# Kernel tuning notes

Hardware: AMD Instinct MI355X
Metric: run time of the kernel (lower is better)

Reference implementation:

```python
import jax, jax.numpy as jnp
import numpy as np

MSA_DIM = 256
N_HEADS = 8
HEAD_DIM = MSA_DIM // N_HEADS
PAIR_DIM = 128
SCALE = 1.0 / float(np.sqrt(HEAD_DIM))


def setup_inputs() -> dict:
    key = jax.random.key(0)
    ks = jax.random.split(key, 7)
    B, S, L = 1, 128, 384
    return {
        "msa": jax.random.normal(ks[0], (B, S, L, MSA_DIM), dtype=jnp.float32),
        "pair": jax.random.normal(ks[1], (B, L, L, PAIR_DIM), dtype=jnp.float32),
        "Wq": jax.random.normal(ks[2], (MSA_DIM, MSA_DIM), dtype=jnp.float32) * 0.02,
        "Wk": jax.random.normal(ks[3], (MSA_DIM, MSA_DIM), dtype=jnp.float32) * 0.02,
        "Wv": jax.random.normal(ks[4], (MSA_DIM, MSA_DIM), dtype=jnp.float32) * 0.02,
        "Wo": jax.random.normal(ks[5], (MSA_DIM, MSA_DIM), dtype=jnp.float32) * 0.02,
        "Wpb": jax.random.normal(ks[6], (N_HEADS, PAIR_DIM), dtype=jnp.float32) * 0.02,
    }


def reference(msa, pair, Wq, Wk, Wv, Wo, Wpb):
    B, S, L, D = msa.shape
    H, hd = N_HEADS, HEAD_DIM
    # projections (nn.Linear: y = x @ W.T), split heads -> (B,S,H,L,hd)
    q = (msa @ Wq.T).reshape(B, S, L, H, hd)
    k = (msa @ Wk.T).reshape(B, S, L, H, hd)
    v = (msa @ Wv.T).reshape(B, S, L, H, hd)
    # NOTE: faithful to the original forward — pair_bias is computed but the
    # Triton kernel performs plain flash attention, so the bias is NOT added.
    _pair_bias = jnp.einsum('bijp,hp->bhij', pair, Wpb)  # dead code, as in source
    # attention logits per MSA row: (B,S,H,L,L)
    scores = jnp.einsum('bslhd,bsmhd->bshlm', q, k) * SCALE
    attn = jax.nn.softmax(scores, axis=-1)
    out = jnp.einsum('bshlm,bsmhd->bslhd', attn, v).reshape(B, S, L, D)
    return out @ Wo.T
```

## Files before the change

### kernel.cpp

```cpp
#include <hip/hip_runtime.h>
#include <stdint.h>

typedef unsigned short u16;
typedef __bf16 bf16x8 __attribute__((ext_vector_type(8)));
typedef short s16x4 __attribute__((ext_vector_type(4)));
typedef float f32x4 __attribute__((ext_vector_type(4)));

#define QKV_STRIDE 12288

__device__ __forceinline__ u16 f2bf(float x) {
    unsigned int u = __float_as_uint(x);
    u += 0x7fffu + ((u >> 16) & 1u);
    return (u16)(u >> 16);
}
__device__ __forceinline__ float bf2f(u16 h) {
    return __uint_as_float(((unsigned int)h) << 16);
}

__device__ __forceinline__ void async_copy16(const u16* g, u16* l) {
    __builtin_amdgcn_global_load_lds(
        (const __attribute__((address_space(1))) unsigned int*)g,
        (__attribute__((address_space(3))) unsigned int*)l, 16, 0, 0);
}

static __device__ __forceinline__ f32x4 pv_mfma(s16x4 a, s16x4 b, f32x4 c) {
#if __has_builtin(__builtin_amdgcn_mfma_f32_16x16x16bf16_1k)
    return __builtin_amdgcn_mfma_f32_16x16x16bf16_1k(a, b, c, 0, 0, 0);
#else
    union { s16x4 h[2]; bf16x8 v; } ua, ub;
    s16x4 zz = {0, 0, 0, 0};
    ua.h[0] = a; ua.h[1] = zz;
    ub.h[0] = b; ub.h[1] = zz;
    return __builtin_amdgcn_mfma_f32_16x16x32_bf16(ua.v, ub.v, c, 0, 0, 0);
#endif
}

__global__ void prep(const float* __restrict__ msa,
                     const float* __restrict__ Wq, const float* __restrict__ Wk,
                     const float* __restrict__ Wv, const float* __restrict__ Wo,
                     u16* __restrict__ msa_bf, u16* __restrict__ Wqkv,
                     u16* __restrict__ Woh, u16* __restrict__ Wol) {
    int b = blockIdx.x;
    if (b < 12288) {
        int i = b * 256 + threadIdx.x;
        float4 v = ((const float4*)msa)[i];
        ushort4 o;
        o.x = f2bf(v.x); o.y = f2bf(v.y); o.z = f2bf(v.z); o.w = f2bf(v.w);
        ((ushort4*)msa_bf)[i] = o;
    } else {
        int i = (b - 12288) * 256 + threadIdx.x;
        Wqkv[i]          = f2bf(Wq[i]);
        Wqkv[65536 + i]  = f2bf(Wk[i]);
        Wqkv[131072 + i] = f2bf(Wv[i]);
        float w = Wo[i];
        u16 hi = f2bf(w);
        Woh[i] = hi;
        Wol[i] = f2bf(w - bf2f(hi));
    }
}

__launch_bounds__(256, 2)
__global__ void qkv_gemm(const u16* __restrict__ A, const u16* __restrict__ W,
                         u16* __restrict__ Qb, u16* __restrict__ Kb, u16* __restrict__ VTb) {
    __shared__ __align__(16) u16 As[128 * 32];
    __shared__ __align__(16) u16 Bs[128 * 32];
    const int tid = threadIdx.x;
    const int tm = blockIdx.x % 384, tn = blockIdx.x / 384;
    const bool trans = (tn < 4);
    const int lane = tid & 63, wave = tid >> 6;
    const int lm = lane & 15, lq = lane >> 4;
    const int wm = (wave >> 1) * 64, wn = (wave & 1) * 64;
    const float CEXPF = 0.17677669529663687f * 1.4426950408889634f;
    f32x4 acc[4][4] = {};

    const int srow = wave * 16 + (lane >> 2);
    const int scol = (lane & 3) * 8;
    u16* ldsA0 = &As[wave * 512 + lane * 8];
    u16* ldsA1 = &As[2048 + wave * 512 + lane * 8];
    u16* ldsB0 = &Bs[wave * 512 + lane * 8];
    u16* ldsB1 = &Bs[2048 + wave * 512 + lane * 8];
    const u16* gA0 = &A[(tm * 128 + srow) * 256 + scol];
    const u16* gA1 = &A[(tm * 128 + 64 + srow) * 256 + scol];
    const u16* gB0 = &W[(tn * 128 + srow) * 256 + scol];
    const u16* gB1 = &W[(tn * 128 + 64 + srow) * 256 + scol];

    for (int k0 = 0; k0 < 256; k0 += 32) {
        async_copy16(gA0 + k0, ldsA0);
        async_copy16(gA1 + k0, ldsA1);
        async_copy16(gB0 + k0, ldsB0);
        async_copy16(gB1 + k0, ldsB1);
        __syncthreads();
        const u16* Xs = trans ? Bs : As;
        const u16* Ys = trans ? As : Bs;
        bf16x8 xf[4], yf[4];
        #pragma unroll
        for (int i = 0; i < 4; ++i)
            xf[i] = *(const bf16x8*)&Xs[(wm + i * 16 + lm) * 32 + lq * 8];
        #pragma unroll
        for (int j = 0; j < 4; ++j)
            yf[j] = *(const bf16x8*)&Ys[(wn + j * 16 + lm) * 32 + lq * 8];
        #pragma unroll
        for (int i = 0; i < 4; ++i)
            #pragma unroll
            for (int j = 0; j < 4; ++j)
                acc[i][j] = __builtin_amdgcn_mfma_f32_16x16x32_bf16(xf[i], yf[j], acc[i][j], 0, 0, 0);
        __syncthreads();
    }

    if (trans) {
        #pragma unroll
        for (int i = 0; i < 4; ++i) {
            int F0 = tn * 128 + wm + i * 16 + lq * 4;
            int which = F0 >> 8;
            int h = (F0 >> 5) & 7, d0 = F0 & 31;
            u16* dst = which ? Kb : Qb;
            float scale = which ? 1.0f : CEXPF;
            #pragma unroll
            for (int j = 0; j < 4; ++j) {
                int R = tm * 128 + wn + j * 16 + lm;
                int s = R / 384, l = R - s * 384;
                ushort4 o;
                o.x = f2bf(acc[i][j][0] * scale);
                o.y = f2bf(acc[i][j][1] * scale);
                o.z = f2bf(acc[i][j][2] * scale);
                o.w = f2bf(acc[i][j][3] * scale);
                *(ushort4*)&dst[((s * 8 + h) * 384 + l) * 32 + d0] = o;
            }
        }
    } else {
        #pragma unroll
        for (int j = 0; j < 4; ++j) {
            int F = tn * 128 + wn + j * 16 + lm;
            int h = (F >> 5) & 7, d = F & 31;
            #pragma unroll
            for (int i = 0; i < 4; ++i) {
                int R0 = tm * 128 + wm + i * 16 + lq * 4;
                int s = R0 / 384, l0 = R0 - s * 384;
                ushort4 o;
                o.x = f2bf(acc[i][j][0]);
                o.y = f2bf(acc[i][j][1]);
                o.z = f2bf(acc[i][j][2]);
                o.w = f2bf(acc[i][j][3]);
                *(ushort4*)&VTb[((s * 8 + h) * 32 + d) * 384 + l0] = o;
            }
        }
    }
}

__launch_bounds__(256, 6)
__global__ void msa_attention(const u16* __restrict__ Qb, const u16* __restrict__ Kb,
                              const u16* __restrict__ VTb,
                              u16* __restrict__ Ahi, u16* __restrict__ Alo) {
    __shared__ __align__(16) u16 Vt[32 * 392];
    const int tid = threadIdx.x;
    const int bid = blockIdx.x;
    const int sh = bid / 3, lpart = bid - sh * 3;
    const int s = sh >> 3, h = sh & 7;
    const u16* Qg = Qb + (size_t)sh * QKV_STRIDE;
    const u16* Kg = Kb + (size_t)sh * QKV_STRIDE;
    const u16* Vg = VTb + (size_t)sh * QKV_STRIDE;

    for (int i = tid; i < 1536; i += 256) {
        int d = i / 48, c = i - d * 48;
        *(uint4*)&Vt[d * 392 + c * 8] = *(const uint4*)&Vg[d * 384 + c * 8];
    }

    const int lane = tid & 63, wave = tid >> 6;
    const int lm = lane & 15, lq = lane >> 4;

    bf16x8 aq[2];
    #pragma unroll
    for (int it = 0; it < 2; ++it) {
        int l = lpart * 128 + (wave * 2 + it) * 16 + lm;
        aq[it] = *(const bf16x8*)&Qg[l * 32 + lq * 8];
    }
    __syncthreads();

    f32x4 o[2][2] = {};
    f32x4 lacc[2] = {};
    const s16x4 ones = {(short)0x3F80, (short)0x3F80, (short)0x3F80, (short)0x3F80};

    for (int n0 = 0; n0 < 384; n0 += 32) {
        bf16x8 kf0 = *(const bf16x8*)&Kg[(n0 + lm) * 32 + lq * 8];
        bf16x8 kf1 = *(const bf16x8*)&Kg[(n0 + 16 + lm) * 32 + lq * 8];
        s16x4 vf00 = *(const s16x4*)&Vt[lm * 392 + n0 + lq * 4];
        s16x4 vf01 = *(const s16x4*)&Vt[lm * 392 + n0 + 16 + lq * 4];
        s16x4 vf10 = *(const s16x4*)&Vt[(16 + lm) * 392 + n0 + lq * 4];
        s16x4 vf11 = *(const s16x4*)&Vt[(16 + lm) * 392 + n0 + 16 + lq * 4];
        #pragma unroll
        for (int it = 0; it < 2; ++it) {
            f32x4 z = {0.f, 0.f, 0.f, 0.f};
            f32x4 s0 = __builtin_amdgcn_mfma_f32_16x16x32_bf16(kf0, aq[it], z, 0, 0, 0);
            f32x4 s1 = __builtin_amdgcn_mfma_f32_16x16x32_bf16(kf1, aq[it], z, 0, 0, 0);
            float p0[4], p1[4];
            #pragma unroll
            for (int r = 0; r < 4; ++r) {
                p0[r] = __builtin_amdgcn_exp2f(s0[r]);
                p1[r] = __builtin_amdgcn_exp2f(s1[r]);
            }
            union { s16x4 v; uint2 u; } pk0, pk1;
            pk0.u.x = __builtin_amdgcn_perm(__float_as_uint(p0[1]), __float_as_uint(p0[0]), 0x07060302u);
            pk0.u.y = __builtin_amdgcn_perm(__float_as_uint(p0[3]), __float_as_uint(p0[2]), 0x07060302u);
            pk1.u.x = __builtin_amdgcn_perm(__float_as_uint(p1[1]), __float_as_uint(p1[0]), 0x07060302u);
            pk1.u.y = __builtin_amdgcn_perm(__float_as_uint(p1[3]), __float_as_uint(p1[2]), 0x07060302u);
            o[it][0] = pv_mfma(vf00, pk0.v, o[it][0]);
            o[it][0] = pv_mfma(vf01, pk1.v, o[it][0]);
            o[it][1] = pv_mfma(vf10, pk0.v, o[it][1]);
            o[it][1] = pv_mfma(vf11, pk1.v, o[it][1]);
            lacc[it] = pv_mfma(ones, pk0.v, lacc[it]);
            lacc[it] = pv_mfma(ones, pk1.v, lacc[it]);
        }
    }

    #pragma unroll
    for (int it = 0; it < 2; ++it) {
        float inv = __builtin_amdgcn_rcpf(lacc[it][0]);
        int l = lpart * 128 + (wave * 2 + it) * 16 + lm;
        int base = (s * 384 + l) * 256 + h * 32 + lq * 4;
        #pragma unroll
        for (int dt = 0; dt < 2; ++dt) {
            ushort4 oh, ol;
            float x0 = o[it][dt][0] * inv, x1 = o[it][dt][1] * inv;
            float x2 = o[it][dt][2] * inv, x3 = o[it][dt][3] * inv;
            oh.x = f2bf(x0); ol.x = f2bf(x0 - bf2f(oh.x));
            oh.y = f2bf(x1); ol.y = f2bf(x1 - bf2f(oh.y));
            oh.z = f2bf(x2); ol.z = f2bf(x2 - bf2f(oh.z));
            oh.w = f2bf(x3); ol.w = f2bf(x3 - bf2f(oh.w));
            *(ushort4*)&Ahi[base + dt * 16] = oh;
            *(ushort4*)&Alo[base + dt * 16] = ol;
        }
    }
}

__launch_bounds__(256, 2)
__global__ void out_gemm(const u16* __restrict__ Ahi, const u16* __restrict__ Alo,
                         const u16* __restrict__ Woh, const u16* __restrict__ Wol,
                         float* __restrict__ out) {
    __shared__ __align__(16) u16 Ah[128 * 32], Al[128 * 32], Bh[128 * 32], Bl[128 * 32];
    const int tid = threadIdx.x;
    const int tm = blockIdx.x % 384, tn = blockIdx.x / 384;
    const int lane = tid & 63, wave = tid >> 6;
    const int lm = lane & 15, lq = lane >> 4;
    const int wm = (wave >> 1) * 64, wn = (wave & 1) * 64;
    f32x4 acc[4][4] = {};

    const int srow = wave * 16 + (lane >> 2);
    const int scol = (lane & 3) * 8;
    const int lo0 = wave * 512 + lane * 8, lo1 = 2048 + wave * 512 + lane * 8;
    const u16* gAh0 = &Ahi[(tm * 128 + srow) * 256 + scol];
    const u16* gAh1 = &Ahi[(tm * 128 + 64 + srow) * 256 + scol];
    const u16* gAl0 = &Alo[(tm * 128 + srow) * 256 + scol];
    const u16* gAl1 = &Alo[(tm * 128 + 64 + srow) * 256 + scol];
    const u16* gBh0 = &Woh[(tn * 128 + srow) * 256 + scol];
    const u16* gBh1 = &Woh[(tn * 128 + 64 + srow) * 256 + scol];
    const u16* gBl0 = &Wol[(tn * 128 + srow) * 256 + scol];
    const u16* gBl1 = &Wol[(tn * 128 + 64 + srow) * 256 + scol];

    for (int k0 = 0; k0 < 256; k0 += 32) {
        async_copy16(gAh0 + k0, &Ah[lo0]);
        async_copy16(gAh1 + k0, &Ah[lo1]);
        async_copy16(gAl0 + k0, &Al[lo0]);
        async_copy16(gAl1 + k0, &Al[lo1]);
        async_copy16(gBh0 + k0, &Bh[lo0]);
        async_copy16(gBh1 + k0, &Bh[lo1]);
        async_copy16(gBl0 + k0, &Bl[lo0]);
        async_copy16(gBl1 + k0, &Bl[lo1]);
        __syncthreads();
        bf16x8 whf[4], wlf[4], ahf[4], alf[4];
        #pragma unroll
        for (int i = 0; i < 4; ++i) {
            whf[i] = *(const bf16x8*)&Bh[(wm + i * 16 + lm) * 32 + lq * 8];
            wlf[i] = *(const bf16x8*)&Bl[(wm + i * 16 + lm) * 32 + lq * 8];
        }
        #pragma unroll
        for (int j = 0; j < 4; ++j) {
            ahf[j] = *(const bf16x8*)&Ah[(wn + j * 16 + lm) * 32 + lq * 8];
            alf[j] = *(const bf16x8*)&Al[(wn + j * 16 + lm) * 32 + lq * 8];
        }
        #pragma unroll
        for (int i = 0; i < 4; ++i)
            #pragma unroll
            for (int j = 0; j < 4; ++j) {
                acc[i][j] = __builtin_amdgcn_mfma_f32_16x16x32_bf16(whf[i], alf[j], acc[i][j], 0, 0, 0);
                acc[i][j] = __builtin_amdgcn_mfma_f32_16x16x32_bf16(wlf[i], ahf[j], acc[i][j], 0, 0, 0);
                acc[i][j] = __builtin_amdgcn_mfma_f32_16x16x32_bf16(whf[i], ahf[j], acc[i][j], 0, 0, 0);
            }
        __syncthreads();
    }
    #pragma unroll
    for (int i = 0; i < 4; ++i) {
        int F0 = tn * 128 + wm + i * 16 + lq * 4;
        #pragma unroll
        for (int j = 0; j < 4; ++j) {
            int R = tm * 128 + wn + j * 16 + lm;
            *(f32x4*)&out[R * 256 + F0] = acc[i][j];
        }
    }
}

extern "C" void kernel_launch(void* const* d_in, const int* in_sizes, int n_in,
                              void* d_out, int out_size, void* d_ws, size_t ws_size,
                              hipStream_t stream) {
    const float* msa = (const float*)d_in[0];
    const float* Wq = (const float*)d_in[2];
    const float* Wk = (const float*)d_in[3];
    const float* Wv = (const float*)d_in[4];
    const float* Wo = (const float*)d_in[5];
    char* ws = (char*)d_ws;
    u16* msa_bf = (u16*)(ws + 0);
    u16* Qb     = (u16*)(ws + 25165824);
    u16* Kb     = (u16*)(ws + 50331648);
    u16* VTb    = (u16*)(ws + 75497472);
    u16* Ahi    = (u16*)(ws + 100663296);
    u16* Alo    = (u16*)(ws + 125829120);
    u16* Wqkv   = (u16*)(ws + 150994944);
    u16* Woh    = (u16*)(ws + 151388160);
    u16* Wol    = (u16*)(ws + 151519232);
    float* out  = (float*)d_out;

    hipLaunchKernelGGL(prep, dim3(12544), dim3(256), 0, stream, msa, Wq, Wk, Wv, Wo,
                       msa_bf, Wqkv, Woh, Wol);
    hipLaunchKernelGGL(qkv_gemm, dim3(2304), dim3(256), 0, stream, msa_bf, Wqkv, Qb, Kb, VTb);
    hipLaunchKernelGGL(msa_attention, dim3(3072), dim3(256), 0, stream, Qb, Kb, VTb, Ahi, Alo);
    hipLaunchKernelGGL(out_gemm, dim3(768), dim3(256), 0, stream, Ahi, Alo, Woh, Wol, out);
}
```

Measured before the change: 264.8 us.

## Drop attention low-precision split, load weights directly to registers, swizzle LDS tiles

The attention output is now stored only as a single bf16 value, with no hi/lo split. This halves the attention write traffic and the out_gemm A-operand reads, and drops one MFMA per tile in out_gemm. Both GEMMs now stage only the activation tile in LDS, using a 64-wide K step and an XOR-swizzled layout to avoid bank conflicts. Weight fragments are loaded straight from global memory into registers. The attention kernel double-buffers the K and V fragments across the unrolled key loop and lowers its occupancy hint from 6 to 4. Accuracy drops slightly because the attention output residual is no longer kept.

```diff
diff --git a/kernel.cpp b/kernel.cpp
--- a/kernel.cpp
+++ b/kernel.cpp
@@ -62,48 +62,53 @@
 __launch_bounds__(256, 2)
 __global__ void qkv_gemm(const u16* __restrict__ A, const u16* __restrict__ W,
                          u16* __restrict__ Qb, u16* __restrict__ Kb, u16* __restrict__ VTb) {
-    __shared__ __align__(16) u16 As[128 * 32];
-    __shared__ __align__(16) u16 Bs[128 * 32];
+    __shared__ __align__(16) u16 As[128 * 64];
     const int tid = threadIdx.x;
     const int tm = blockIdx.x % 384, tn = blockIdx.x / 384;
     const bool trans = (tn < 4);
     const int lane = tid & 63, wave = tid >> 6;
     const int lm = lane & 15, lq = lane >> 4;
+    const int lm7 = lm & 7;
     const int wm = (wave >> 1) * 64, wn = (wave & 1) * 64;
     const float CEXPF = 0.17677669529663687f * 1.4426950408889634f;
     f32x4 acc[4][4] = {};
 
-    const int srow = wave * 16 + (lane >> 2);
-    const int scol = (lane & 3) * 8;
-    u16* ldsA0 = &As[wave * 512 + lane * 8];
-    u16* ldsA1 = &As[2048 + wave * 512 + lane * 8];
-    u16* ldsB0 = &Bs[wave * 512 + lane * 8];
-    u16* ldsB1 = &Bs[2048 + wave * 512 + lane * 8];
-    const u16* gA0 = &A[(tm * 128 + srow) * 256 + scol];
-    const u16* gA1 = &A[(tm * 128 + 64 + srow) * 256 + scol];
-    const u16* gB0 = &W[(tn * 128 + srow) * 256 + scol];
-    const u16* gB1 = &W[(tn * 128 + 64 + srow) * 256 + scol];
-
-    for (int k0 = 0; k0 < 256; k0 += 32) {
-        async_copy16(gA0 + k0, ldsA0);
-        async_copy16(gA1 + k0, ldsA1);
-        async_copy16(gB0 + k0, ldsB0);
-        async_copy16(gB1 + k0, ldsB1);
+    const int srow = wave * 8 + (lane >> 3);
+    const int schunk = (lane & 7) ^ (lane >> 3);
+    u16* ldsd[4]; const u16* gsrc[4];
+    #pragma unroll
+    for (int j = 0; j < 4; ++j) {
+        ldsd[j] = &As[j * 2048 + wave * 512 + lane * 8];
+        gsrc[j] = &A[(tm * 128 + j * 32 + srow) * 256 + schunk * 8];
+    }
+    const int rbm = trans ? wn : wm;
+    const int rbg = tn * 128 + (trans ? wm : wn);
+
+    for (int k0 = 0; k0 < 256; k0 += 64) {
+        #pragma unroll
+        for (int j = 0; j < 4; ++j) async_copy16(gsrc[j] + k0, ldsd[j]);
+        bf16x8 wf[4][2];
+        #pragma unroll
+        for (int x = 0; x < 4; ++x)
+            #pragma unroll
+            for (int kk = 0; kk < 2; ++kk)
+                wf[x][kk] = *(const bf16x8*)&W[(rbg + x * 16 + lm) * 256 + k0 + kk * 32 + lq * 8];
         __syncthreads();
-        const u16* Xs = trans ? Bs : As;
-        const u16* Ys = trans ? As : Bs;
-        bf16x8 xf[4], yf[4];
-        #pragma unroll
-        for (int i = 0; i < 4; ++i)
-            xf[i] = *(const bf16x8*)&Xs[(wm + i * 16 + lm) * 32 + lq * 8];
-        #pragma unroll
-        for (int j = 0; j < 4; ++j)
-            yf[j] = *(const bf16x8*)&Ys[(wn + j * 16 + lm) * 32 + lq * 8];
-        #pragma unroll
-        for (int i = 0; i < 4; ++i)
-            #pragma unroll
-            for (int j = 0; j < 4; ++j)
-                acc[i][j] = __builtin_amdgcn_mfma_f32_16x16x32_bf16(xf[i], yf[j], acc[i][j], 0, 0, 0);
+        bf16x8 mf[4][2];
+        #pragma unroll
+        for (int x = 0; x < 4; ++x)
+            #pragma unroll
+            for (int kk = 0; kk < 2; ++kk)
+                mf[x][kk] = *(const bf16x8*)&As[(rbm + x * 16 + lm) * 64 + ((kk * 4 + lq) ^ lm7) * 8];
+        #pragma unroll
+        for (int kk = 0; kk < 2; ++kk)
+            #pragma unroll
+            for (int i = 0; i < 4; ++i)
+                #pragma unroll
+                for (int j = 0; j < 4; ++j)
+                    acc[i][j] = __builtin_amdgcn_mfma_f32_16x16x32_bf16(
+                        trans ? wf[i][kk] : mf[i][kk],
+                        trans ? mf[j][kk] : wf[j][kk], acc[i][j], 0, 0, 0);
         __syncthreads();
     }
 
@@ -147,10 +152,9 @@
     }
 }
 
-__launch_bounds__(256, 6)
+__launch_bounds__(256, 4)
 __global__ void msa_attention(const u16* __restrict__ Qb, const u16* __restrict__ Kb,
-                              const u16* __restrict__ VTb,
-                              u16* __restrict__ Ahi, u16* __restrict__ Alo) {
+                              const u16* __restrict__ VTb, u16* __restrict__ Ahi) {
     __shared__ __align__(16) u16 Vt[32 * 392];
     const int tid = threadIdx.x;
     const int bid = blockIdx.x;
@@ -174,24 +178,38 @@
         int l = lpart * 128 + (wave * 2 + it) * 16 + lm;
         aq[it] = *(const bf16x8*)&Qg[l * 32 + lq * 8];
     }
+
+    bf16x8 kf0[2], kf1[2];
+    kf0[0] = *(const bf16x8*)&Kg[lm * 32 + lq * 8];
+    kf1[0] = *(const bf16x8*)&Kg[(16 + lm) * 32 + lq * 8];
     __syncthreads();
+    s16x4 vf[2][4];
+    vf[0][0] = *(const s16x4*)&Vt[lm * 392 + lq * 4];
+    vf[0][1] = *(const s16x4*)&Vt[lm * 392 + 16 + lq * 4];
+    vf[0][2] = *(const s16x4*)&Vt[(16 + lm) * 392 + lq * 4];
+    vf[0][3] = *(const s16x4*)&Vt[(16 + lm) * 392 + 16 + lq * 4];
 
     f32x4 o[2][2] = {};
     f32x4 lacc[2] = {};
     const s16x4 ones = {(short)0x3F80, (short)0x3F80, (short)0x3F80, (short)0x3F80};
 
-    for (int n0 = 0; n0 < 384; n0 += 32) {
-        bf16x8 kf0 = *(const bf16x8*)&Kg[(n0 + lm) * 32 + lq * 8];
-        bf16x8 kf1 = *(const bf16x8*)&Kg[(n0 + 16 + lm) * 32 + lq * 8];
-        s16x4 vf00 = *(const s16x4*)&Vt[lm * 392 + n0 + lq * 4];
-        s16x4 vf01 = *(const s16x4*)&Vt[lm * 392 + n0 + 16 + lq * 4];
-        s16x4 vf10 = *(const s16x4*)&Vt[(16 + lm) * 392 + n0 + lq * 4];
-        s16x4 vf11 = *(const s16x4*)&Vt[(16 + lm) * 392 + n0 + 16 + lq * 4];
+    #pragma unroll
+    for (int t = 0; t < 12; ++t) {
+        const int cur = t & 1, nxt = cur ^ 1;
+        if (t < 11) {
+            const int nn = (t + 1) * 32;
+            kf0[nxt] = *(const bf16x8*)&Kg[(nn + lm) * 32 + lq * 8];
+            kf1[nxt] = *(const bf16x8*)&Kg[(nn + 16 + lm) * 32 + lq * 8];
+            vf[nxt][0] = *(const s16x4*)&Vt[lm * 392 + nn + lq * 4];
+            vf[nxt][1] = *(const s16x4*)&Vt[lm * 392 + nn + 16 + lq * 4];
+            vf[nxt][2] = *(const s16x4*)&Vt[(16 + lm) * 392 + nn + lq * 4];
+            vf[nxt][3] = *(const s16x4*)&Vt[(16 + lm) * 392 + nn + 16 + lq * 4];
+        }
         #pragma unroll
         for (int it = 0; it < 2; ++it) {
             f32x4 z = {0.f, 0.f, 0.f, 0.f};
-            f32x4 s0 = __builtin_amdgcn_mfma_f32_16x16x32_bf16(kf0, aq[it], z, 0, 0, 0);
-            f32x4 s1 = __builtin_amdgcn_mfma_f32_16x16x32_bf16(kf1, aq[it], z, 0, 0, 0);
+            f32x4 s0 = __builtin_amdgcn_mfma_f32_16x16x32_bf16(kf0[cur], aq[it], z, 0, 0, 0);
+            f32x4 s1 = __builtin_amdgcn_mfma_f32_16x16x32_bf16(kf1[cur], aq[it], z, 0, 0, 0);
             float p0[4], p1[4];
             #pragma unroll
             for (int r = 0; r < 4; ++r) {
@@ -203,10 +221,10 @@
             pk0.u.y = __builtin_amdgcn_perm(__float_as_uint(p0[3]), __float_as_uint(p0[2]), 0x07060302u);
             pk1.u.x = __builtin_amdgcn_perm(__float_as_uint(p1[1]), __float_as_uint(p1[0]), 0x07060302u);
             pk1.u.y = __builtin_amdgcn_perm(__float_as_uint(p1[3]), __float_as_uint(p1[2]), 0x07060302u);
-            o[it][0] = pv_mfma(vf00, pk0.v, o[it][0]);
-            o[it][0] = pv_mfma(vf01, pk1.v, o[it][0]);
-            o[it][1] = pv_mfma(vf10, pk0.v, o[it][1]);
-            o[it][1] = pv_mfma(vf11, pk1.v, o[it][1]);
+            o[it][0] = pv_mfma(vf[cur][0], pk0.v, o[it][0]);
+            o[it][0] = pv_mfma(vf[cur][1], pk1.v, o[it][0]);
+            o[it][1] = pv_mfma(vf[cur][2], pk0.v, o[it][1]);
+            o[it][1] = pv_mfma(vf[cur][3], pk1.v, o[it][1]);
             lacc[it] = pv_mfma(ones, pk0.v, lacc[it]);
             lacc[it] = pv_mfma(ones, pk1.v, lacc[it]);
         }
@@ -219,72 +237,66 @@
         int base = (s * 384 + l) * 256 + h * 32 + lq * 4;
         #pragma unroll
         for (int dt = 0; dt < 2; ++dt) {
-            ushort4 oh, ol;
-            float x0 = o[it][dt][0] * inv, x1 = o[it][dt][1] * inv;
-            float x2 = o[it][dt][2] * inv, x3 = o[it][dt][3] * inv;
-            oh.x = f2bf(x0); ol.x = f2bf(x0 - bf2f(oh.x));
-            oh.y = f2bf(x1); ol.y = f2bf(x1 - bf2f(oh.y));
-            oh.z = f2bf(x2); ol.z = f2bf(x2 - bf2f(oh.z));
-            oh.w = f2bf(x3); ol.w = f2bf(x3 - bf2f(oh.w));
+            ushort4 oh;
+            oh.x = f2bf(o[it][dt][0] * inv);
+            oh.y = f2bf(o[it][dt][1] * inv);
+            oh.z = f2bf(o[it][dt][2] * inv);
+            oh.w = f2bf(o[it][dt][3] * inv);
             *(ushort4*)&Ahi[base + dt * 16] = oh;
-            *(ushort4*)&Alo[base + dt * 16] = ol;
         }
     }
 }
 
 __launch_bounds__(256, 2)
-__global__ void out_gemm(const u16* __restrict__ Ahi, const u16* __restrict__ Alo,
+__global__ void out_gemm(const u16* __restrict__ Ahi,
                          const u16* __restrict__ Woh, const u16* __restrict__ Wol,
                          float* __restrict__ out) {
-    __shared__ __align__(16) u16 Ah[128 * 32], Al[128 * 32], Bh[128 * 32], Bl[128 * 32];
+    __shared__ __align__(16) u16 As[128 * 64];
     const int tid = threadIdx.x;
     const int tm = blockIdx.x % 384, tn = blockIdx.x / 384;
     const int lane = tid & 63, wave = tid >> 6;
     const int lm = lane & 15, lq = lane >> 4;
+    const int lm7 = lm & 7;
     const int wm = (wave >> 1) * 64, wn = (wave & 1) * 64;
     f32x4 acc[4][4] = {};
 
-    const int srow = wave * 16 + (lane >> 2);
-    const int scol = (lane & 3) * 8;
-    const int lo0 = wave * 512 + lane * 8, lo1 = 2048 + wave * 512 + lane * 8;
-    const u16* gAh0 = &Ahi[(tm * 128 + srow) * 256 + scol];
-    const u16* gAh1 = &Ahi[(tm * 128 + 64 + srow) * 256 + scol];
-    const u16* gAl0 = &Alo[(tm * 128 + srow) * 256 + scol];
-    const u16* gAl1 = &Alo[(tm * 128 + 64 + srow) * 256 + scol];
-    const u16* gBh0 = &Woh[(tn * 128 + srow) * 256 + scol];
-    const u16* gBh1 = &Woh[(tn * 128 + 64 + srow) * 256 + scol];
-    const u16* gBl0 = &Wol[(tn * 128 + srow) * 256 + scol];
-    const u16* gBl1 = &Wol[(tn * 128 + 64 + srow) * 256 + scol];
-
-    for (int k0 = 0; k0 < 256; k0 += 32) {
-        async_copy16(gAh0 + k0, &Ah[lo0]);
-        async_copy16(gAh1 + k0, &Ah[lo1]);
-        async_copy16(gAl0 + k0, &Al[lo0]);
-        async_copy16(gAl1 + k0, &Al[lo1]);
-        async_copy16(gBh0 + k0, &Bh[lo0]);
-        async_copy16(gBh1 + k0, &Bh[lo1]);
-        async_copy16(gBl0 + k0, &Bl[lo0]);
-        async_copy16(gBl1 + k0, &Bl[lo1]);
+    const int srow = wave * 8 + (lane >> 3);
+    const int schunk = (lane & 7) ^ (lane >> 3);
+    u16* ldsd[4]; const u16* gsrc[4];
+    #pragma unroll
+    for (int j = 0; j < 4; ++j) {
+        ldsd[j] = &As[j * 2048 + wave * 512 + lane * 8];
+        gsrc[j] = &Ahi[(tm * 128 + j * 32 + srow) * 256 + schunk * 8];
+    }
+
+    for (int k0 = 0; k0 < 256; k0 += 64) {
+        #pragma unroll
+        for (int j = 0; j < 4; ++j) async_copy16(gsrc[j] + k0, ldsd[j]);
+        bf16x8 whf[4][2], wlf[4][2];
+        #pragma unroll
+        for (int i = 0; i < 4; ++i)
+            #pragma unroll
+            for (int kk = 0; kk < 2; ++kk) {
+                int off = (tn * 128 + wm + i * 16 + lm) * 256 + k0 + kk * 32 + lq * 8;
+                whf[i][kk] = *(const bf16x8*)&Woh[off];
+                wlf[i][kk] = *(const bf16x8*)&Wol[off];
+            }
         __syncthreads();
-        bf16x8 whf[4], wlf[4], ahf[4], alf[4];
-        #pragma unroll
-        for (int i = 0; i < 4; ++i) {
-            whf[i] = *(const bf16x8*)&Bh[(wm + i * 16 + lm) * 32 + lq * 8];
-            wlf[i] = *(const bf16x8*)&Bl[(wm + i * 16 + lm) * 32 + lq * 8];
-        }
-        #pragma unroll
-        for (int j = 0; j < 4; ++j) {
-            ahf[j] = *(const bf16x8*)&Ah[(wn + j * 16 + lm) * 32 + lq * 8];
-            alf[j] = *(const bf16x8*)&Al[(wn + j * 16 + lm) * 32 + lq * 8];
-        }
-        #pragma unroll
-        for (int i = 0; i < 4; ++i)
-            #pragma unroll
-            for (int j = 0; j < 4; ++j) {
-                acc[i][j] = __builtin_amdgcn_mfma_f32_16x16x32_bf16(whf[i], alf[j], acc[i][j], 0, 0, 0);
-                acc[i][j] = __builtin_amdgcn_mfma_f32_16x16x32_bf16(wlf[i], ahf[j], acc[i][j], 0, 0, 0);
-                acc[i][j] = __builtin_amdgcn_mfma_f32_16x16x32_bf16(whf[i], ahf[j], acc[i][j], 0, 0, 0);
-            }
+        bf16x8 af[4][2];
+        #pragma unroll
+        for (int j = 0; j < 4; ++j)
+            #pragma unroll
+            for (int kk = 0; kk < 2; ++kk)
+                af[j][kk] = *(const bf16x8*)&As[(wn + j * 16 + lm) * 64 + ((kk * 4 + lq) ^ lm7) * 8];
+        #pragma unroll
+        for (int kk = 0; kk < 2; ++kk)
+            #pragma unroll
+            for (int i = 0; i < 4; ++i)
+                #pragma unroll
+                for (int j = 0; j < 4; ++j) {
+                    acc[i][j] = __builtin_amdgcn_mfma_f32_16x16x32_bf16(wlf[i][kk], af[j][kk], acc[i][j], 0, 0, 0);
+                    acc[i][j] = __builtin_amdgcn_mfma_f32_16x16x32_bf16(whf[i][kk], af[j][kk], acc[i][j], 0, 0, 0);
+                }
         __syncthreads();
     }
     #pragma unroll
@@ -312,7 +324,6 @@
     u16* Kb     = (u16*)(ws + 50331648);
     u16* VTb    = (u16*)(ws + 75497472);
     u16* Ahi    = (u16*)(ws + 100663296);
-    u16* Alo    = (u16*)(ws + 125829120);
     u16* Wqkv   = (u16*)(ws + 150994944);
     u16* Woh    = (u16*)(ws + 151388160);
     u16* Wol    = (u16*)(ws + 151519232);
@@ -321,6 +332,6 @@
     hipLaunchKernelGGL(prep, dim3(12544), dim3(256), 0, stream, msa, Wq, Wk, Wv, Wo,
                        msa_bf, Wqkv, Woh, Wol);
     hipLaunchKernelGGL(qkv_gemm, dim3(2304), dim3(256), 0, stream, msa_bf, Wqkv, Qb, Kb, VTb);
-    hipLaunchKernelGGL(msa_attention, dim3(3072), dim3(256), 0, stream, Qb, Kb, VTb, Ahi, Alo);
-    hipLaunchKernelGGL(out_gemm, dim3(768), dim3(256), 0, stream, Ahi, Alo, Woh, Wol, out);
-}
+    hipLaunchKernelGGL(msa_attention, dim3(3072), dim3(256), 0, stream, Qb, Kb, VTb, Ahi);
+    hipLaunchKernelGGL(out_gemm, dim3(768), dim3(256), 0, stream, Ahi, Woh, Wol, out);
+}
```

Measured after the change: 272.0 us. +2.7%, slower.
